# Optimization experiments

Hardware: AMD Instinct MI355X
Metric: run time of the kernel (lower is better)

The kernel has to match this reference:

```python
import jax, jax.numpy as jnp
import numpy as np
from jax import lax

# Dims from LSTMTagger class constants
B, S, LP = 1024, 128, 14       # sentences, words/sentence, padded chars/word
K, CE, WE, Lf = 3, 6, 10, 4    # char window, char emb, word emb, cnn filters
H, V, A, T = 6, 50000, 100, 135  # lstm hidden, vocab, alphabet, tagset
D = WE + Lf                     # lstm input dim = 14
LW = LP - K + 1                 # conv windows per word = 12


def setup_inputs() -> dict:
    key = jax.random.key(0)
    ks = jax.random.split(key, 14)
    n = lambda k, shp: jax.random.normal(k, shp, dtype=jnp.float32) * 0.1
    inp = {
        "word_idx": jax.random.randint(ks[0], (B, S), 0, V, dtype=jnp.int32),
        "char_idx": jax.random.randint(ks[1], (B, S, LP), 0, A, dtype=jnp.int32),
        "word_emb": n(ks[2], (V, WE)),
        "char_emb": n(ks[3], (A, CE)),
        "Wc": n(ks[4], (Lf, K * CE)),   # Conv1d(1, l, K*CE) weight, squeezed
        "bc": n(ks[5], (Lf,)),
        "Wih_f": n(ks[6], (4 * H, D)),
        "Whh_f": n(ks[7], (4 * H, H)),
        "b_f": n(ks[8], (4 * H,)),      # b_ih + b_hh fused (equivalent)
        "Wih_b": n(ks[9], (4 * H, D)),
        "Whh_b": n(ks[10], (4 * H, H)),
        "b_b": n(ks[11], (4 * H,)),
        "Wt": n(ks[12], (T, 2 * H)),
        "bt": n(ks[13], (T,)),
    }
    return inp


def _lstm_scan(xs, Wih, Whh, b):
    # xs: [S, B, D] -> hs: [S, B, H]; torch gate order i, f, g, o
    h0 = jnp.zeros((xs.shape[1], H), xs.dtype)

    def step(carry, xt):
        h, c = carry
        g = xt @ Wih.T + h @ Whh.T + b
        i, f, gg, o = jnp.split(g, 4, axis=-1)
        c = jax.nn.sigmoid(f) * c + jax.nn.sigmoid(i) * jnp.tanh(gg)
        h = jax.nn.sigmoid(o) * jnp.tanh(c)
        return (h, c), h

    _, hs = lax.scan(step, (h0, h0), xs)
    return hs


def reference(word_emb, char_emb, Wc, bc, Wih_f, Whh_f, b_f,
              Wih_b, Whh_b, b_b, Wt, bt, word_idx, char_idx):
    # per-word char CNN: sliding K-char windows, flatten, linear, max-pool
    ce = char_emb[char_idx]                              # [B,S,LP,CE]
    windows = jnp.concatenate([ce[:, :, i:i + LW] for i in range(K)], axis=-1)  # [B,S,LW,K*CE]
    phi = jnp.einsum('bswk,lk->bswl', windows, Wc) + bc  # [B,S,LW,Lf]
    char_repr = phi.max(axis=2)                          # [B,S,Lf]

    we = word_emb[word_idx]                              # [B,S,WE]
    x = jnp.concatenate([we, char_repr], axis=-1)        # [B,S,D]

    xs = x.transpose(1, 0, 2)                            # [S,B,D]
    hf = _lstm_scan(xs, Wih_f, Whh_f, b_f)               # forward direction
    hb = _lstm_scan(xs[::-1], Wih_b, Whh_b, b_b)[::-1]   # backward direction
    out = jnp.concatenate([hf, hb], axis=-1).transpose(1, 0, 2)  # [B,S,2H]

    tag_space = out @ Wt.T + bt                          # [B,S,T]
    return jax.nn.log_softmax(tag_space, axis=-1)
```

## Files before the change

kernel.cpp:

```cpp
#include <hip/hip_runtime.h>

#define B_   1024
#define S_   128
#define LP_  14
#define K_   3
#define CE_  6
#define WE_  10
#define LF_  4
#define H_   6
#define D_   14
#define T_   135
#define LW_  12
#define V_   50000
#define A_   100
#define NSEQ (B_ * 2)

static __device__ __forceinline__ float fsigm(float x) {
    return __frcp_rn(1.0f + __expf(-x));
}
static __device__ __forceinline__ float ftanh(float x) {
    return fmaf(2.0f, __frcp_rn(1.0f + __expf(-2.0f * x)), -1.0f);
}

__global__ __launch_bounds__(256) void k_e(
    const int* __restrict__ word_idx, const int* __restrict__ char_idx,
    const float* __restrict__ word_emb, const float* __restrict__ char_emb,
    const float* __restrict__ Wc, const float* __restrict__ bc,
    const float* __restrict__ Wih_f, const float* __restrict__ b_f,
    const float* __restrict__ Wih_b, const float* __restrict__ b_b,
    float* __restrict__ gbuf)
{
    __shared__ float s_ce[A_ * CE_];
    __shared__ float s_wc[LF_ * K_ * CE_];
    __shared__ float s_bc[LF_];
    int t = threadIdx.x;
    for (int e = t; e < A_ * CE_; e += 256) s_ce[e] = char_emb[e];
    if (t < LF_ * K_ * CE_) s_wc[t] = Wc[t];
    if (t < LF_) s_bc[t] = bc[t];
    __syncthreads();

    int wid = blockIdx.x * 256 + t;
    int s = wid >> 10;
    int b = wid & 1023;
    int w = b * S_ + s;

    const int2* ci2 = (const int2*)(char_idx + (size_t)w * LP_);
    int idxs[LP_];
    #pragma unroll
    for (int p = 0; p < 7; ++p) {
        int2 v = ci2[p];
        idxs[2 * p] = v.x; idxs[2 * p + 1] = v.y;
    }
    float ce[LP_][CE_];
    #pragma unroll
    for (int p = 0; p < LP_; ++p) {
        int idx = idxs[p];
        idx = idx < 0 ? 0 : (idx >= A_ ? A_ - 1 : idx);
        #pragma unroll
        for (int c = 0; c < CE_; ++c) ce[p][c] = s_ce[idx * CE_ + c];
    }
    float x[D_];
    #pragma unroll
    for (int l = 0; l < LF_; ++l) {
        float acc[LW_];
        float bl = s_bc[l];
        #pragma unroll
        for (int q = 0; q < LW_; ++q) acc[q] = bl;
        #pragma unroll
        for (int kk = 0; kk < K_; ++kk) {
            #pragma unroll
            for (int c = 0; c < CE_; ++c) {
                float wv_ = s_wc[l * (K_ * CE_) + kk * CE_ + c];
                #pragma unroll
                for (int q = 0; q < LW_; ++q) acc[q] = fmaf(ce[q + kk][c], wv_, acc[q]);
            }
        }
        float m = acc[0];
        #pragma unroll
        for (int q = 1; q < LW_; ++q) m = fmaxf(m, acc[q]);
        x[WE_ + l] = m;
    }
    int wi = word_idx[w];
    wi = wi < 0 ? 0 : (wi >= V_ ? V_ - 1 : wi);
    const float2* wep = (const float2*)(word_emb + (size_t)wi * WE_);
    #pragma unroll
    for (int c = 0; c < WE_ / 2; ++c) {
        float2 v = wep[c];
        x[2 * c] = v.x; x[2 * c + 1] = v.y;
    }

    float* dst = gbuf + ((size_t)s * NSEQ + 2 * b) * 24;
    {
        float g[24];
        #pragma unroll
        for (int r = 0; r < 24; ++r) {
            float a = b_f[r];
            #pragma unroll
            for (int k = 0; k < D_; ++k) a = fmaf(Wih_f[r * D_ + k], x[k], a);
            g[r] = a;
        }
        #pragma unroll
        for (int q = 0; q < 6; ++q)
            ((float4*)dst)[q] = make_float4(g[4 * q], g[4 * q + 1], g[4 * q + 2], g[4 * q + 3]);
    }
    {
        float g[24];
        #pragma unroll
        for (int r = 0; r < 24; ++r) {
            float a = b_b[r];
            #pragma unroll
            for (int k = 0; k < D_; ++k) a = fmaf(Wih_b[r * D_ + k], x[k], a);
            g[r] = a;
        }
        #pragma unroll
        for (int q = 0; q < 6; ++q)
            ((float4*)(dst + 24))[q] = make_float4(g[4 * q], g[4 * q + 1], g[4 * q + 2], g[4 * q + 3]);
    }
}

__global__ __launch_bounds__(64) void k_l(
    const float* __restrict__ Whh_f, const float* __restrict__ Whh_b,
    const float* __restrict__ gbuf, float* __restrict__ hbuf)
{
    int lane = threadIdx.x;
    int grp  = lane >> 3;
    int u8   = lane & 7;
    bool act = (u8 < H_);
    int u    = act ? u8 : (H_ - 1);
    int seq  = blockIdx.x * 8 + grp;
    int b    = seq >> 1;
    int dir  = seq & 1;

    const float* Whh = dir ? Whh_b : Whh_f;
    float w0[H_], w1[H_], w2[H_], w3[H_];
    #pragma unroll
    for (int k = 0; k < H_; ++k) {
        w0[k] = Whh[(0 * H_ + u) * H_ + k];
        w1[k] = Whh[(1 * H_ + u) * H_ + k];
        w2[k] = Whh[(2 * H_ + u) * H_ + k];
        w3[k] = Whh[(3 * H_ + u) * H_ + k];
    }

    const float* gp = gbuf + ((size_t)(dir ? S_ - 1 : 0) * NSEQ + (size_t)seq) * 24 + u;
    long gstride = (dir ? -1L : 1L) * (long)(NSEQ * 24);

#define LD4(dstv, p) { dstv[0] = (p)[0]; dstv[1] = (p)[6]; dstv[2] = (p)[12]; dstv[3] = (p)[18]; }

    float a0[4], a1[4], p0[4] = {0,0,0,0}, p1[4] = {0,0,0,0};
    LD4(a0, gp);
    LD4(a1, gp + gstride);
    const float* gpn = gp + 2 * gstride;

    float h[H_];
    #pragma unroll
    for (int k = 0; k < H_; ++k) h[k] = 0.f;
    float c = 0.f;
    int gb = grp << 3;

#define STEP(gv, sidx)                                                          \
    {                                                                           \
        float ai = gv[0], af = gv[1], ag = gv[2], ao = gv[3];                   \
        _Pragma("unroll")                                                       \
        for (int k = 0; k < H_; ++k) {                                          \
            ai = fmaf(w0[k], h[k], ai);                                         \
            af = fmaf(w1[k], h[k], af);                                         \
            ag = fmaf(w2[k], h[k], ag);                                         \
            ao = fmaf(w3[k], h[k], ao);                                         \
        }                                                                       \
        float si = fsigm(ai), sf = fsigm(af), so = fsigm(ao), tg = ftanh(ag);   \
        c = fmaf(sf, c, si * tg);                                               \
        float hu = so * ftanh(c);                                               \
        int se = dir ? (S_ - 1 - (sidx)) : (sidx);                              \
        if (act) hbuf[((size_t)b * S_ + se) * 12 + dir * H_ + u] = hu;          \
        _Pragma("unroll")                                                       \
        for (int k = 0; k < H_; ++k) h[k] = __shfl(hu, gb + k, 64);             \
    }

    for (int s = 0; s < S_; s += 2) {
        if (s + 2 < S_) { LD4(p0, gpn); gpn += gstride; }
        STEP(a0, s);
        if (s + 3 < S_) { LD4(p1, gpn); gpn += gstride; }
        STEP(a1, s + 1);
        #pragma unroll
        for (int q = 0; q < 4; ++q) { a0[q] = p0[q]; a1[q] = p1[q]; }
    }
#undef STEP
#undef LD4
}

__global__ __launch_bounds__(256) void k_p(
    const float* __restrict__ hbuf,
    const float* __restrict__ Wt, const float* __restrict__ bt,
    float* __restrict__ out)
{
    __shared__ float s_hb[64 * 12];
    int t = threadIdx.x;
    int ib = blockIdx.x * 64;
    {
        const float4* src = (const float4*)(hbuf + (size_t)ib * 12);
        float4* dst = (float4*)s_hb;
        if (t < 192) dst[t] = src[t];
    }
    __syncthreads();

    int lane = t & 63, wv = t >> 6;
    bool has2 = (lane < T_ - 128);
    int t2c = has2 ? (lane + 128) : (T_ - 1);

    float wA[12], wB[12], wC[12];
    #pragma unroll
    for (int jj = 0; jj < 12; ++jj) {
        wA[jj] = Wt[lane * 12 + jj];
        wB[jj] = Wt[(lane + 64) * 12 + jj];
        wC[jj] = Wt[t2c * 12 + jj];
    }
    float bA = bt[lane], bB = bt[lane + 64], bC = bt[t2c];

    int it0 = wv * 16;
    #pragma unroll 4
    for (int k = 0; k < 16; ++k) {
        int it = it0 + k;
        const float4* h4 = (const float4*)(s_hb + it * 12);
        float4 a0 = h4[0], a1 = h4[1], a2 = h4[2];
        float hv[12] = {a0.x, a0.y, a0.z, a0.w, a1.x, a1.y, a1.z, a1.w, a2.x, a2.y, a2.z, a2.w};
        float y0 = bA, y1 = bB, y2 = bC;
        #pragma unroll
        for (int jj = 0; jj < 12; ++jj) {
            y0 = fmaf(hv[jj], wA[jj], y0);
            y1 = fmaf(hv[jj], wB[jj], y1);
            y2 = fmaf(hv[jj], wC[jj], y2);
        }
        float ss = __expf(y0) + __expf(y1) + (has2 ? __expf(y2) : 0.0f);
        #pragma unroll
        for (int mk = 1; mk < 64; mk <<= 1) ss += __shfl_xor(ss, mk, 64);
        float ls = __logf(ss);
        float* op = out + (size_t)(ib + it) * T_;
        op[lane]      = y0 - ls;
        op[lane + 64] = y1 - ls;
        if (has2) op[lane + 128] = y2 - ls;
    }
}

extern "C" void kernel_launch(void* const* d_in, const int* in_sizes, int n_in,
                              void* d_out, int out_size, void* d_ws, size_t ws_size,
                              hipStream_t stream)
{
    const int* word_idx = (const int*)d_in[0];
    const int* char_idx = (const int*)d_in[1];
    const float* word_emb = (const float*)d_in[2];
    const float* char_emb = (const float*)d_in[3];
    const float* Wc    = (const float*)d_in[4];
    const float* bc    = (const float*)d_in[5];
    const float* Wih_f = (const float*)d_in[6];
    const float* Whh_f = (const float*)d_in[7];
    const float* b_f   = (const float*)d_in[8];
    const float* Wih_b = (const float*)d_in[9];
    const float* Whh_b = (const float*)d_in[10];
    const float* b_b   = (const float*)d_in[11];
    const float* Wt    = (const float*)d_in[12];
    const float* bt    = (const float*)d_in[13];

    const size_t hbuf_fl = (size_t)B_ * S_ * 12;
    const size_t gbuf_fl = (size_t)S_ * NSEQ * 24;

    float* hbuf = (float*)d_ws;
    float* gbuf;
    if (ws_size >= (hbuf_fl + gbuf_fl) * sizeof(float)) {
        gbuf = (float*)d_ws + hbuf_fl;
    } else {
        gbuf = (float*)d_out;
    }

    k_e<<<(B_ * S_) / 256, 256, 0, stream>>>(word_idx, char_idx, word_emb, char_emb,
                                             Wc, bc, Wih_f, b_f, Wih_b, b_b, gbuf);
    k_l<<<NSEQ / 8, 64, 0, stream>>>(Whh_f, Whh_b, gbuf, hbuf);
    k_p<<<(B_ * S_) / 64, 256, 0, stream>>>(hbuf, Wt, bt, (float*)d_out);
}
```

Baseline: 192.0 us.

## Interleave LSTM gate preactivations per unit, deepen prefetch, use DPP wave reduction

The embedding kernel now writes input-gate preactivations interleaved per hidden unit (i,f,g,o contiguous), so each LSTM lane loads one float4 per step instead of four strided scalars. The recurrence kernel keeps an 8-deep register prefetch ring of these float4 loads and advances the hbuf output pointer incrementally. The log-softmax reduction swaps the shuffle-xor butterfly for DPP row operations plus readlane. These changes aim to hide global load latency on the serial recurrence and cut reduction cost, at the price of more registers and a DPP sequence that depends on the hardware's exact row semantics.

Result: faster. 181.9 us (-5.3%).

```diff
diff --git a/kernel.cpp b/kernel.cpp
--- a/kernel.cpp
+++ b/kernel.cpp
@@ -22,6 +22,18 @@
     return fmaf(2.0f, __frcp_rn(1.0f + __expf(-2.0f * x)), -1.0f);
 }
 
+static __device__ __forceinline__ float wave_sum64(float s) {
+    int v = __float_as_int(s);
+    float f;
+    f = __int_as_float(__builtin_amdgcn_update_dpp(0, v, 0xB1, 0xF, 0xF, true));  s += f; v = __float_as_int(s);
+    f = __int_as_float(__builtin_amdgcn_update_dpp(0, v, 0x4E, 0xF, 0xF, true));  s += f; v = __float_as_int(s);
+    f = __int_as_float(__builtin_amdgcn_update_dpp(0, v, 0x141, 0xF, 0xF, true)); s += f; v = __float_as_int(s);
+    f = __int_as_float(__builtin_amdgcn_update_dpp(0, v, 0x140, 0xF, 0xF, true)); s += f; v = __float_as_int(s);
+    f = __int_as_float(__builtin_amdgcn_update_dpp(0, v, 0x142, 0xA, 0xF, true)); s += f; v = __float_as_int(s);
+    f = __int_as_float(__builtin_amdgcn_update_dpp(0, v, 0x143, 0xC, 0xF, true)); s += f; v = __float_as_int(s);
+    return __int_as_float(__builtin_amdgcn_readlane(v, 63));
+}
+
 __global__ __launch_bounds__(256) void k_e(
     const int* __restrict__ word_idx, const int* __restrict__ char_idx,
     const float* __restrict__ word_emb, const float* __restrict__ char_emb,
@@ -100,8 +112,8 @@
             g[r] = a;
         }
         #pragma unroll
-        for (int q = 0; q < 6; ++q)
-            ((float4*)dst)[q] = make_float4(g[4 * q], g[4 * q + 1], g[4 * q + 2], g[4 * q + 3]);
+        for (int u = 0; u < H_; ++u)
+            ((float4*)dst)[u] = make_float4(g[u], g[H_ + u], g[2 * H_ + u], g[3 * H_ + u]);
     }
     {
         float g[24];
@@ -113,8 +125,8 @@
             g[r] = a;
         }
         #pragma unroll
-        for (int q = 0; q < 6; ++q)
-            ((float4*)(dst + 24))[q] = make_float4(g[4 * q], g[4 * q + 1], g[4 * q + 2], g[4 * q + 3]);
+        for (int u = 0; u < H_; ++u)
+            ((float4*)(dst + 24))[u] = make_float4(g[u], g[H_ + u], g[2 * H_ + u], g[3 * H_ + u]);
     }
 }
 
@@ -130,6 +142,7 @@
     int seq  = blockIdx.x * 8 + grp;
     int b    = seq >> 1;
     int dir  = seq & 1;
+    int gb   = grp << 3;
 
     const float* Whh = dir ? Whh_b : Whh_f;
     float w0[H_], w1[H_], w2[H_], w3[H_];
@@ -141,51 +154,47 @@
         w3[k] = Whh[(3 * H_ + u) * H_ + k];
     }
 
-    const float* gp = gbuf + ((size_t)(dir ? S_ - 1 : 0) * NSEQ + (size_t)seq) * 24 + u;
-    long gstride = (dir ? -1L : 1L) * (long)(NSEQ * 24);
-
-#define LD4(dstv, p) { dstv[0] = (p)[0]; dstv[1] = (p)[6]; dstv[2] = (p)[12]; dstv[3] = (p)[18]; }
-
-    float a0[4], a1[4], p0[4] = {0,0,0,0}, p1[4] = {0,0,0,0};
-    LD4(a0, gp);
-    LD4(a1, gp + gstride);
-    const float* gpn = gp + 2 * gstride;
+    const long gstride = (dir ? -1L : 1L) * (long)(NSEQ * 24);
+    const float* gp = gbuf + ((size_t)(dir ? S_ - 1 : 0) * NSEQ + (size_t)seq) * 24 + u * 4;
+
+    float4 pf[8];
+    #pragma unroll
+    for (int j = 0; j < 8; ++j) pf[j] = *(const float4*)(gp + j * gstride);
+    const float* gn = gp + 8 * gstride;
+
+    float* hp = hbuf + ((size_t)b * S_ + (size_t)(dir ? S_ - 1 : 0)) * 12 + dir * H_ + u;
+    const int hstride = dir ? -12 : 12;
 
     float h[H_];
     #pragma unroll
     for (int k = 0; k < H_; ++k) h[k] = 0.f;
     float c = 0.f;
-    int gb = grp << 3;
-
-#define STEP(gv, sidx)                                                          \
-    {                                                                           \
-        float ai = gv[0], af = gv[1], ag = gv[2], ao = gv[3];                   \
-        _Pragma("unroll")                                                       \
-        for (int k = 0; k < H_; ++k) {                                          \
-            ai = fmaf(w0[k], h[k], ai);                                         \
-            af = fmaf(w1[k], h[k], af);                                         \
-            ag = fmaf(w2[k], h[k], ag);                                         \
-            ao = fmaf(w3[k], h[k], ao);                                         \
-        }                                                                       \
-        float si = fsigm(ai), sf = fsigm(af), so = fsigm(ao), tg = ftanh(ag);   \
-        c = fmaf(sf, c, si * tg);                                               \
-        float hu = so * ftanh(c);                                               \
-        int se = dir ? (S_ - 1 - (sidx)) : (sidx);                              \
-        if (act) hbuf[((size_t)b * S_ + se) * 12 + dir * H_ + u] = hu;          \
-        _Pragma("unroll")                                                       \
-        for (int k = 0; k < H_; ++k) h[k] = __shfl(hu, gb + k, 64);             \
-    }
-
-    for (int s = 0; s < S_; s += 2) {
-        if (s + 2 < S_) { LD4(p0, gpn); gpn += gstride; }
-        STEP(a0, s);
-        if (s + 3 < S_) { LD4(p1, gpn); gpn += gstride; }
-        STEP(a1, s + 1);
-        #pragma unroll
-        for (int q = 0; q < 4; ++q) { a0[q] = p0[q]; a1[q] = p1[q]; }
-    }
-#undef STEP
-#undef LD4
+
+    for (int m = 0; m < S_; m += 8) {
+        #pragma unroll
+        for (int j = 0; j < 8; ++j) {
+            float4 g4 = pf[j];
+            if (m + 8 + j < S_) {
+                pf[j] = *(const float4*)gn;
+                gn += gstride;
+            }
+            float ai = g4.x, af = g4.y, ag = g4.z, ao = g4.w;
+            #pragma unroll
+            for (int k = 0; k < H_; ++k) {
+                ai = fmaf(w0[k], h[k], ai);
+                af = fmaf(w1[k], h[k], af);
+                ag = fmaf(w2[k], h[k], ag);
+                ao = fmaf(w3[k], h[k], ao);
+            }
+            float si = fsigm(ai), sf = fsigm(af), so = fsigm(ao), tg = ftanh(ag);
+            c = fmaf(sf, c, si * tg);
+            float hu = so * ftanh(c);
+            if (act) *hp = hu;
+            hp += hstride;
+            #pragma unroll
+            for (int k = 0; k < H_; ++k) h[k] = __shfl(hu, gb + k, 64);
+        }
+    }
 }
 
 __global__ __launch_bounds__(256) void k_p(
@@ -231,9 +240,7 @@
             y2 = fmaf(hv[jj], wC[jj], y2);
         }
         float ss = __expf(y0) + __expf(y1) + (has2 ? __expf(y2) : 0.0f);
-        #pragma unroll
-        for (int mk = 1; mk < 64; mk <<= 1) ss += __shfl_xor(ss, mk, 64);
-        float ls = __logf(ss);
+        float ls = __logf(wave_sum64(ss));
         float* op = out + (size_t)(ib + it) * T_;
         op[lane]      = y0 - ls;
         op[lane + 64] = y1 - ls;
```
